# Kernel tuning notes

Measured on AMD Instinct MI355X. Metric: run time of the kernel, lower is better.

## Reference

```python
import jax, jax.numpy as jnp
import numpy as np

EMBED_DIM = 1024
NUM_HEADS = 16
D_K = EMBED_DIM // NUM_HEADS


def setup_inputs() -> dict:
    key = jax.random.key(0)
    ks = jax.random.split(key, 5)
    s = 1.0 / np.sqrt(EMBED_DIM)  # roughly match nn.Linear init scale
    return {
        "x": jax.random.normal(ks[0], (2, 2048, EMBED_DIM), dtype=jnp.float32),
        "wq": jax.random.normal(ks[1], (EMBED_DIM, EMBED_DIM), dtype=jnp.float32) * s,
        "wk": jax.random.normal(ks[2], (EMBED_DIM, EMBED_DIM), dtype=jnp.float32) * s,
        "wv": jax.random.normal(ks[3], (EMBED_DIM, EMBED_DIM), dtype=jnp.float32) * s,
        "wo": jax.random.normal(ks[4], (EMBED_DIM, EMBED_DIM), dtype=jnp.float32) * s,
    }


def reference(x, wq, wk, wv, wo):
    b, s, e = x.shape
    # nn.Linear(bias=False): y = x @ W.T
    def split_heads(t):
        return t.reshape(b, s, NUM_HEADS, D_K).transpose(0, 2, 1, 3)  # [b,h,s,d]
    q = split_heads(x @ wq.T)
    k = split_heads(x @ wk.T)
    v = split_heads(x @ wv.T)
    scores = jnp.einsum("bhqd,bhkd->bhqk", q, k) / jnp.sqrt(jnp.float32(D_K))
    attn = jax.nn.softmax(scores, axis=-1)
    out = jnp.einsum("bhqk,bhkd->bhqd", attn, v)  # [b,h,s,d]
    out = out.transpose(0, 2, 1, 3).reshape(b, s, e)
    return out @ wo.T
```

## Files before the change

kernel.cpp:

```cpp
#include <hip/hip_runtime.h>
#include <stdint.h>

typedef unsigned short u16;
typedef float f32x4 __attribute__((ext_vector_type(4)));
typedef __bf16 bf16x8 __attribute__((ext_vector_type(8)));

__device__ __forceinline__ u16 f2bf(float f) {
  union { float f; uint32_t u; } c; c.f = f;
  uint32_t u = c.u;
  u += 0x7fffu + ((u >> 16) & 1u);
  return (u16)(u >> 16);
}

#define GLOAD_LDS16(g, l)                                                              \
  __builtin_amdgcn_global_load_lds((__attribute__((address_space(1))) void*)(g),       \
                                   (__attribute__((address_space(3))) void*)(l), 16, 0, 0)

__global__ __launch_bounds__(256) void cvt_all(const float* __restrict__ x,
                                               const float* __restrict__ wq,
                                               const float* __restrict__ wk,
                                               const float* __restrict__ wv,
                                               const float* __restrict__ wo,
                                               u16* __restrict__ xb,
                                               u16* __restrict__ wqkvb,
                                               u16* __restrict__ wob) {
  int bx = blockIdx.x;
  const float* src;
  u16* dst;
  int i;
  if (bx < 4096) {
    src = x; dst = xb; i = bx * 256 + threadIdx.x;
  } else {
    int r = bx - 4096;
    int w = r >> 10;
    i = (r & 1023) * 256 + threadIdx.x;
    if (w == 0)      { src = wq; dst = wqkvb; }
    else if (w == 1) { src = wk; dst = wqkvb + 1048576; }
    else if (w == 2) { src = wv; dst = wqkvb + 2097152; }
    else             { src = wo; dst = wob; }
  }
  const float4 v = ((const float4*)src)[i];
  ushort4 o;
  o.x = f2bf(v.x); o.y = f2bf(v.y); o.z = f2bf(v.z); o.w = f2bf(v.w);
  ((ushort4*)dst)[i] = o;
}

__global__ __launch_bounds__(256) void gemm_qkv(const u16* __restrict__ A,
                                                const u16* __restrict__ B,
                                                u16* __restrict__ QKb,
                                                u16* __restrict__ Vt) {
  const int K = 1024;
  __shared__ __align__(16) u16 sA[128 * 32];
  __shared__ __align__(16) u16 sB[128 * 32];
  const int tid = threadIdx.x;
  const int lane = tid & 63;
  const int wave = tid >> 6;
  const int quad = lane >> 4, l16 = lane & 15;
  const int wm = (wave >> 1) * 64, wn = (wave & 1) * 64;
  const int bm = blockIdx.y * 128, bn = blockIdx.x * 128;

  const int ar = tid >> 2;
  const int ac = (tid & 3) * 8;

  f32x4 acc[4][4];
#pragma unroll
  for (int i = 0; i < 4; i++)
#pragma unroll
    for (int j = 0; j < 4; j++) acc[i][j] = (f32x4){0.f, 0.f, 0.f, 0.f};

  const u16* pA0 = A + (size_t)(bm + ar) * K + ac;
  const u16* pA1 = A + (size_t)(bm + 64 + ar) * K + ac;
  const u16* pB0 = B + (size_t)(bn + ar) * K + ac;
  const u16* pB1 = B + (size_t)(bn + 64 + ar) * K + ac;

  for (int k0 = 0; k0 < K; k0 += 32) {
    GLOAD_LDS16(pA0 + k0, (char*)sA + tid * 16);
    GLOAD_LDS16(pA1 + k0, (char*)sA + 4096 + tid * 16);
    GLOAD_LDS16(pB0 + k0, (char*)sB + tid * 16);
    GLOAD_LDS16(pB1 + k0, (char*)sB + 4096 + tid * 16);
    __syncthreads();
    bf16x8 af[4], bfr[4];
#pragma unroll
    for (int mt = 0; mt < 4; mt++)
      af[mt] = *(const bf16x8*)&sA[(wm + mt * 16 + l16) * 32 + quad * 8];
#pragma unroll
    for (int nt = 0; nt < 4; nt++)
      bfr[nt] = *(const bf16x8*)&sB[(wn + nt * 16 + l16) * 32 + quad * 8];
#pragma unroll
    for (int mt = 0; mt < 4; mt++)
#pragma unroll
      for (int nt = 0; nt < 4; nt++)
        acc[mt][nt] = __builtin_amdgcn_mfma_f32_16x16x32_bf16(af[mt], bfr[nt], acc[mt][nt], 0, 0, 0);
    __syncthreads();
  }

  if (blockIdx.x < 16) {
    const float qs = (blockIdx.x < 8) ? 0.125f : 1.0f;
#pragma unroll
    for (int mt = 0; mt < 4; mt++)
#pragma unroll
      for (int nt = 0; nt < 4; nt++)
#pragma unroll
        for (int r = 0; r < 4; r++) {
          int row = bm + wm + mt * 16 + quad * 4 + r;
          int col = bn + wn + nt * 16 + l16;
          QKb[(size_t)row * 2048 + col] = f2bf(acc[mt][nt][r] * qs);
        }
  } else {
#pragma unroll
    for (int mt = 0; mt < 4; mt++)
#pragma unroll
      for (int nt = 0; nt < 4; nt++) {
        int hd = (bn - 2048) + wn + nt * 16 + l16;
        int tok = bm + wm + mt * 16 + quad * 4;
        ushort4 o;
        o.x = f2bf(acc[mt][nt][0]);
        o.y = f2bf(acc[mt][nt][1]);
        o.z = f2bf(acc[mt][nt][2]);
        o.w = f2bf(acc[mt][nt][3]);
        *(ushort4*)&Vt[(size_t)hd * 4096 + tok] = o;
      }
  }
}

__global__ __launch_bounds__(256, 2) void attn_fwd(const u16* __restrict__ QKb,
                                                   const u16* __restrict__ Vt,
                                                   u16* __restrict__ O) {
  const int qt = blockIdx.x, h = blockIdx.y, b = blockIdx.z;
  const int tid = threadIdx.x;
  const int lane = tid & 63;
  const int wave = tid >> 6;
  const int quad = lane >> 4, l16 = lane & 15;
  const int qh = wave >> 1;
  const int kvh = wave & 1;

  __shared__ __align__(16) u16 sK[2][128 * 64];
  __shared__ __align__(16) u16 sV[2][64 * 128];
  __shared__ __align__(16) u16 sQP[8192];

  const int tok0 = b * 2048;
  const int q0 = qt * 128;
  const int colh = h * 64;

#pragma unroll
  for (int k2 = 0; k2 < 4; k2++) {
    int c = k2 * 256 + tid;
    int row = c >> 3, c8 = (c & 7) ^ (row & 7);
    GLOAD_LDS16(QKb + (size_t)(tok0 + q0 + row) * 2048 + colh + c8 * 8,
                (char*)sQP + c * 16);
  }
#pragma unroll
  for (int k2 = 0; k2 < 4; k2++) {
    int c = k2 * 256 + tid;
    int rowk = c >> 3, c8 = (c & 7) ^ (rowk & 7);
    GLOAD_LDS16(QKb + (size_t)(tok0 + rowk) * 2048 + 1024 + colh + c8 * 8,
                (char*)sK[0] + c * 16);
    int rowv = c >> 4, c16 = (c & 15) ^ (rowv & 15);
    GLOAD_LDS16(Vt + (size_t)(colh + rowv) * 4096 + tok0 + c16 * 8,
                (char*)sV[0] + c * 16);
  }
  __syncthreads();

  bf16x8 aq[4][2];
#pragma unroll
  for (int sub = 0; sub < 4; sub++)
#pragma unroll
    for (int kh = 0; kh < 2; kh++) {
      int row = qh * 64 + sub * 16 + l16;
      aq[sub][kh] = *(const bf16x8*)&sQP[row * 64 + (((kh * 4 + quad) ^ (row & 7)) * 8)];
    }
  __syncthreads();

  u16* sP = sQP + wave * 1152;

  f32x4 oacc[4][4];
  float lsum[4][4];
#pragma unroll
  for (int sub = 0; sub < 4; sub++)
#pragma unroll
    for (int nt = 0; nt < 4; nt++) oacc[sub][nt] = (f32x4){0.f, 0.f, 0.f, 0.f};
#pragma unroll
  for (int sub = 0; sub < 4; sub++)
#pragma unroll
    for (int r = 0; r < 4; r++) lsum[sub][r] = 0.f;

  int p = 0;
  for (int it = 0; it < 16; ++it) {
    const int nkv = (it < 15 ? it + 1 : 15) * 128;
#pragma unroll
    for (int k2 = 0; k2 < 4; k2++) {
      int c = k2 * 256 + tid;
      int rowk = c >> 3, c8 = (c & 7) ^ (rowk & 7);
      GLOAD_LDS16(QKb + (size_t)(tok0 + nkv + rowk) * 2048 + 1024 + colh + c8 * 8,
                  (char*)sK[p ^ 1] + c * 16);
      int rowv = c >> 4, c16 = (c & 15) ^ (rowv & 15);
      GLOAD_LDS16(Vt + (size_t)(colh + rowv) * 4096 + tok0 + nkv + c16 * 8,
                  (char*)sV[p ^ 1] + c * 16);
    }

    bf16x8 kf[4][2], vf[4][2];
#pragma unroll
    for (int nt = 0; nt < 4; nt++)
#pragma unroll
      for (int kh = 0; kh < 2; kh++) {
        int rk = kvh * 64 + nt * 16 + l16;
        kf[nt][kh] = *(const bf16x8*)&sK[p][rk * 64 + (((kh * 4 + quad) ^ (rk & 7)) * 8)];
        int rv = nt * 16 + l16;
        vf[nt][kh] = *(const bf16x8*)&sV[p][rv * 128 + (((kvh * 8 + kh * 4 + quad) ^ (rv & 15)) * 8)];
      }

#pragma unroll
    for (int sub = 0; sub < 4; sub++) {
      f32x4 sc[4];
#pragma unroll
      for (int nt = 0; nt < 4; nt++) {
        f32x4 c = (f32x4){0.f, 0.f, 0.f, 0.f};
        c = __builtin_amdgcn_mfma_f32_16x16x32_bf16(aq[sub][0], kf[nt][0], c, 0, 0, 0);
        c = __builtin_amdgcn_mfma_f32_16x16x32_bf16(aq[sub][1], kf[nt][1], c, 0, 0, 0);
        sc[nt] = c;
      }
#pragma unroll
      for (int nt = 0; nt < 4; nt++)
#pragma unroll
        for (int r = 0; r < 4; r++) {
          union { float f; uint32_t u; } cc;
          cc.f = __expf(sc[nt][r]);
          sP[(quad * 4 + r) * 72 + nt * 16 + l16] = (u16)(cc.u >> 16);
          cc.u &= 0xffff0000u;
          lsum[sub][r] += cc.f;
        }
      bf16x8 ap0 = *(const bf16x8*)&sP[l16 * 72 + quad * 8];
      bf16x8 ap1 = *(const bf16x8*)&sP[l16 * 72 + 32 + quad * 8];
#pragma unroll
      for (int nt = 0; nt < 4; nt++) {
        oacc[sub][nt] = __builtin_amdgcn_mfma_f32_16x16x32_bf16(ap0, vf[nt][0], oacc[sub][nt], 0, 0, 0);
        oacc[sub][nt] = __builtin_amdgcn_mfma_f32_16x16x32_bf16(ap1, vf[nt][1], oacc[sub][nt], 0, 0, 0);
      }
    }
    __syncthreads();
    p ^= 1;
  }

#pragma unroll
  for (int sub = 0; sub < 4; sub++)
#pragma unroll
    for (int r = 0; r < 4; r++) {
      float v = lsum[sub][r];
#pragma unroll
      for (int m = 1; m < 16; m <<= 1) v += __shfl_xor(v, m, 64);
      lsum[sub][r] = v;
    }

  float* mO = (float*)sK;
  float* mL = (float*)sV;
  if (kvh == 1) {
#pragma unroll
    for (int sub = 0; sub < 4; sub++)
#pragma unroll
      for (int nt = 0; nt < 4; nt++)
#pragma unroll
        for (int r = 0; r < 4; r++)
          mO[qh * 4096 + (sub * 16 + quad * 4 + r) * 64 + nt * 16 + l16] = oacc[sub][nt][r];
    if (l16 == 0)
#pragma unroll
      for (int sub = 0; sub < 4; sub++)
#pragma unroll
        for (int r = 0; r < 4; r++)
          mL[qh * 64 + sub * 16 + quad * 4 + r] = lsum[sub][r];
  }
  __syncthreads();
  if (kvh == 0) {
#pragma unroll
    for (int sub = 0; sub < 4; sub++)
#pragma unroll
      for (int r = 0; r < 4; r++) {
        int ql = sub * 16 + quad * 4 + r;
        float inv = 1.0f / (lsum[sub][r] + mL[qh * 64 + ql]);
        int row = tok0 + q0 + qh * 64 + ql;
#pragma unroll
        for (int nt = 0; nt < 4; nt++) {
          float o = oacc[sub][nt][r] + mO[qh * 4096 + ql * 64 + nt * 16 + l16];
          O[(size_t)row * 1024 + colh + nt * 16 + l16] = f2bf(o * inv);
        }
      }
  }
}

__global__ __launch_bounds__(256) void gemm_out(const u16* __restrict__ A,
                                                const u16* __restrict__ B,
                                                float* __restrict__ C) {
  const int N = 1024, K = 1024;
  __shared__ __align__(16) u16 sA[128 * 32];
  __shared__ __align__(16) u16 sB[64 * 32];
  const int tid = threadIdx.x;
  const int lane = tid & 63;
  const int wave = tid >> 6;
  const int quad = lane >> 4, l16 = lane & 15;
  const int wm = (wave >> 1) * 64, wn = (wave & 1) * 32;
  const int bm = blockIdx.y * 128, bn = blockIdx.x * 64;
  const int ar = tid >> 2;
  const int ac = (tid & 3) * 8;

  f32x4 acc[4][2];
#pragma unroll
  for (int i = 0; i < 4; i++)
#pragma unroll
    for (int j = 0; j < 2; j++) acc[i][j] = (f32x4){0.f, 0.f, 0.f, 0.f};

  const u16* pA0 = A + (size_t)(bm + ar) * K + ac;
  const u16* pA1 = A + (size_t)(bm + 64 + ar) * K + ac;
  const u16* pB0 = B + (size_t)(bn + ar) * K + ac;

  for (int k0 = 0; k0 < K; k0 += 32) {
    GLOAD_LDS16(pA0 + k0, (char*)sA + tid * 16);
    GLOAD_LDS16(pA1 + k0, (char*)sA + 4096 + tid * 16);
    GLOAD_LDS16(pB0 + k0, (char*)sB + tid * 16);
    __syncthreads();
    bf16x8 af[4], bfr[2];
#pragma unroll
    for (int mt = 0; mt < 4; mt++)
      af[mt] = *(const bf16x8*)&sA[(wm + mt * 16 + l16) * 32 + quad * 8];
#pragma unroll
    for (int nt = 0; nt < 2; nt++)
      bfr[nt] = *(const bf16x8*)&sB[(wn + nt * 16 + l16) * 32 + quad * 8];
#pragma unroll
    for (int mt = 0; mt < 4; mt++)
#pragma unroll
      for (int nt = 0; nt < 2; nt++)
        acc[mt][nt] = __builtin_amdgcn_mfma_f32_16x16x32_bf16(af[mt], bfr[nt], acc[mt][nt], 0, 0, 0);
    __syncthreads();
  }

#pragma unroll
  for (int mt = 0; mt < 4; mt++)
#pragma unroll
    for (int nt = 0; nt < 2; nt++)
#pragma unroll
      for (int r = 0; r < 4; r++) {
        int row = bm + wm + mt * 16 + quad * 4 + r;
        int col = bn + wn + nt * 16 + l16;
        C[(size_t)row * N + col] = acc[mt][nt][r];
      }
}

extern "C" void kernel_launch(void* const* d_in, const int* in_sizes, int n_in,
                              void* d_out, int out_size, void* d_ws, size_t ws_size,
                              hipStream_t stream) {
  const float* x  = (const float*)d_in[0];
  const float* wq = (const float*)d_in[1];
  const float* wk = (const float*)d_in[2];
  const float* wv = (const float*)d_in[3];
  const float* wo = (const float*)d_in[4];
  float* out = (float*)d_out;
  char* ws = (char*)d_ws;
  const size_t MB = 1u << 20;

  u16* xb    = (u16*)(ws);
  u16* wqkvb = (u16*)(ws + 8 * MB);
  u16* wob   = (u16*)(ws + 14 * MB);
  u16* QKb   = (u16*)(ws + 16 * MB);
  u16* Vtb   = (u16*)(ws + 32 * MB);
  u16* Ob    = xb;

  cvt_all<<<8192, 256, 0, stream>>>(x, wq, wk, wv, wo, xb, wqkvb, wob);

  gemm_qkv<<<dim3(24, 32), 256, 0, stream>>>(xb, wqkvb, QKb, Vtb);

  attn_fwd<<<dim3(16, 16, 2), 256, 0, stream>>>(QKb, Vtb, Ob);

  gemm_out<<<dim3(16, 32), 256, 0, stream>>>(Ob, wob, out);
}
```

Baseline: 211.7 us.

## Restructure attention: per-wave query rows, transposed MFMA, register P via shuffles

Rewrites the attention kernel so each wave owns 32 query rows over the full KV range with 64-token KV tiles, and drops the split-KV merge through shared memory. It swaps the MFMA operand order so scores land transposed, packs exp values to bf16 with perm and redistributes them through lane shuffles instead of an LDS round-trip for P. It also shrinks LDS to raise occupancy to 3 blocks, linearizes the grid, and stages output through LDS for 16-byte stores. The cost is more shuffle traffic and more loop iterations with more barriers. The packing step changes bf16 rounding of the row sums slightly.

```diff
diff --git a/kernel.cpp b/kernel.cpp
--- a/kernel.cpp
+++ b/kernel.cpp
@@ -10,6 +10,11 @@
   uint32_t u = c.u;
   u += 0x7fffu + ((u >> 16) & 1u);
   return (u16)(u >> 16);
+}
+
+__device__ __forceinline__ uint32_t pkbf(float a, float b) {
+  union { float f; uint32_t u; } ua, ub; ua.f = a; ub.f = b;
+  return __builtin_amdgcn_perm(ub.u, ua.u, 0x07060302u);
 }
 
 #define GLOAD_LDS16(g, l)                                                              \
@@ -123,20 +128,24 @@
   }
 }
 
-__global__ __launch_bounds__(256, 2) void attn_fwd(const u16* __restrict__ QKb,
+__global__ __launch_bounds__(256, 3) void attn_fwd(const u16* __restrict__ QKb,
                                                    const u16* __restrict__ Vt,
                                                    u16* __restrict__ O) {
-  const int qt = blockIdx.x, h = blockIdx.y, b = blockIdx.z;
+  const int bx = blockIdx.x;
+  const int qt = bx >> 5;
+  const int h  = (bx >> 1) & 15;
+  const int b  = bx & 1;
   const int tid = threadIdx.x;
   const int lane = tid & 63;
   const int wave = tid >> 6;
   const int quad = lane >> 4, l16 = lane & 15;
-  const int qh = wave >> 1;
-  const int kvh = wave & 1;
-
-  __shared__ __align__(16) u16 sK[2][128 * 64];
-  __shared__ __align__(16) u16 sV[2][64 * 128];
-  __shared__ __align__(16) u16 sQP[8192];
+
+  __shared__ __align__(16) u16 smem[24576];
+  u16* sK0 = smem;
+  u16* sK1 = smem + 4096;
+  u16* sV0 = smem + 8192;
+  u16* sV1 = smem + 12288;
+  u16* sQ  = smem + 16384;
 
   const int tok0 = b * 2048;
   const int q0 = qt * 128;
@@ -147,55 +156,56 @@
     int c = k2 * 256 + tid;
     int row = c >> 3, c8 = (c & 7) ^ (row & 7);
     GLOAD_LDS16(QKb + (size_t)(tok0 + q0 + row) * 2048 + colh + c8 * 8,
-                (char*)sQP + c * 16);
-  }
-#pragma unroll
-  for (int k2 = 0; k2 < 4; k2++) {
+                (char*)sQ + c * 16);
+  }
+#pragma unroll
+  for (int k2 = 0; k2 < 2; k2++) {
     int c = k2 * 256 + tid;
-    int rowk = c >> 3, c8 = (c & 7) ^ (rowk & 7);
-    GLOAD_LDS16(QKb + (size_t)(tok0 + rowk) * 2048 + 1024 + colh + c8 * 8,
-                (char*)sK[0] + c * 16);
-    int rowv = c >> 4, c16 = (c & 15) ^ (rowv & 15);
-    GLOAD_LDS16(Vt + (size_t)(colh + rowv) * 4096 + tok0 + c16 * 8,
-                (char*)sV[0] + c * 16);
+    int row = c >> 3, c8 = (c & 7) ^ (row & 7);
+    GLOAD_LDS16(QKb + (size_t)(tok0 + row) * 2048 + 1024 + colh + c8 * 8,
+                (char*)sK0 + c * 16);
+    GLOAD_LDS16(Vt + (size_t)(colh + row) * 4096 + tok0 + c8 * 8,
+                (char*)sV0 + c * 16);
   }
   __syncthreads();
 
-  bf16x8 aq[4][2];
-#pragma unroll
-  for (int sub = 0; sub < 4; sub++)
+  bf16x8 aq[2][2];
+#pragma unroll
+  for (int sub = 0; sub < 2; sub++)
 #pragma unroll
     for (int kh = 0; kh < 2; kh++) {
-      int row = qh * 64 + sub * 16 + l16;
-      aq[sub][kh] = *(const bf16x8*)&sQP[row * 64 + (((kh * 4 + quad) ^ (row & 7)) * 8)];
+      int row = wave * 32 + sub * 16 + l16;
+      aq[sub][kh] = *(const bf16x8*)&sQ[row * 64 + (((kh * 4 + quad) ^ (row & 7)) * 8)];
     }
-  __syncthreads();
-
-  u16* sP = sQP + wave * 1152;
-
-  f32x4 oacc[4][4];
-  float lsum[4][4];
-#pragma unroll
-  for (int sub = 0; sub < 4; sub++)
+
+  f32x4 oacc[2][4];
+  float lsum[2] = {0.f, 0.f};
+#pragma unroll
+  for (int sub = 0; sub < 2; sub++)
 #pragma unroll
     for (int nt = 0; nt < 4; nt++) oacc[sub][nt] = (f32x4){0.f, 0.f, 0.f, 0.f};
-#pragma unroll
-  for (int sub = 0; sub < 4; sub++)
-#pragma unroll
-    for (int r = 0; r < 4; r++) lsum[sub][r] = 0.f;
+
+  const int srcA = ((quad & 1) * 32 + l16);
+  const int srcB = srcA + 16;
+  const bool hiT = (quad >= 2);
 
   int p = 0;
-  for (int it = 0; it < 16; ++it) {
-    const int nkv = (it < 15 ? it + 1 : 15) * 128;
-#pragma unroll
-    for (int k2 = 0; k2 < 4; k2++) {
-      int c = k2 * 256 + tid;
-      int rowk = c >> 3, c8 = (c & 7) ^ (rowk & 7);
-      GLOAD_LDS16(QKb + (size_t)(tok0 + nkv + rowk) * 2048 + 1024 + colh + c8 * 8,
-                  (char*)sK[p ^ 1] + c * 16);
-      int rowv = c >> 4, c16 = (c & 15) ^ (rowv & 15);
-      GLOAD_LDS16(Vt + (size_t)(colh + rowv) * 4096 + tok0 + nkv + c16 * 8,
-                  (char*)sV[p ^ 1] + c * 16);
+  for (int it = 0; it < 32; ++it) {
+    u16* sKc = p ? sK1 : sK0;
+    u16* sVc = p ? sV1 : sV0;
+    if (it < 31) {
+      u16* sKn = p ? sK0 : sK1;
+      u16* sVn = p ? sV0 : sV1;
+      const int nkv = (it + 1) * 64;
+#pragma unroll
+      for (int k2 = 0; k2 < 2; k2++) {
+        int c = k2 * 256 + tid;
+        int row = c >> 3, c8 = (c & 7) ^ (row & 7);
+        GLOAD_LDS16(QKb + (size_t)(tok0 + nkv + row) * 2048 + 1024 + colh + c8 * 8,
+                    (char*)sKn + c * 16);
+        GLOAD_LDS16(Vt + (size_t)(colh + row) * 4096 + tok0 + nkv + c8 * 8,
+                    (char*)sVn + c * 16);
+      }
     }
 
     bf16x8 kf[4][2], vf[4][2];
@@ -203,38 +213,46 @@
     for (int nt = 0; nt < 4; nt++)
 #pragma unroll
       for (int kh = 0; kh < 2; kh++) {
-        int rk = kvh * 64 + nt * 16 + l16;
-        kf[nt][kh] = *(const bf16x8*)&sK[p][rk * 64 + (((kh * 4 + quad) ^ (rk & 7)) * 8)];
-        int rv = nt * 16 + l16;
-        vf[nt][kh] = *(const bf16x8*)&sV[p][rv * 128 + (((kvh * 8 + kh * 4 + quad) ^ (rv & 15)) * 8)];
-      }
-
-#pragma unroll
-    for (int sub = 0; sub < 4; sub++) {
-      f32x4 sc[4];
+        int rr = nt * 16 + l16;
+        int off = rr * 64 + (((kh * 4 + quad) ^ (rr & 7)) * 8);
+        kf[nt][kh] = *(const bf16x8*)&sKc[off];
+        vf[nt][kh] = *(const bf16x8*)&sVc[off];
+      }
+
+#pragma unroll
+    for (int sub = 0; sub < 2; sub++) {
+      f32x4 e[4];
 #pragma unroll
       for (int nt = 0; nt < 4; nt++) {
         f32x4 c = (f32x4){0.f, 0.f, 0.f, 0.f};
-        c = __builtin_amdgcn_mfma_f32_16x16x32_bf16(aq[sub][0], kf[nt][0], c, 0, 0, 0);
-        c = __builtin_amdgcn_mfma_f32_16x16x32_bf16(aq[sub][1], kf[nt][1], c, 0, 0, 0);
-        sc[nt] = c;
-      }
-#pragma unroll
-      for (int nt = 0; nt < 4; nt++)
-#pragma unroll
-        for (int r = 0; r < 4; r++) {
-          union { float f; uint32_t u; } cc;
-          cc.f = __expf(sc[nt][r]);
-          sP[(quad * 4 + r) * 72 + nt * 16 + l16] = (u16)(cc.u >> 16);
-          cc.u &= 0xffff0000u;
-          lsum[sub][r] += cc.f;
-        }
-      bf16x8 ap0 = *(const bf16x8*)&sP[l16 * 72 + quad * 8];
-      bf16x8 ap1 = *(const bf16x8*)&sP[l16 * 72 + 32 + quad * 8];
-#pragma unroll
-      for (int nt = 0; nt < 4; nt++) {
-        oacc[sub][nt] = __builtin_amdgcn_mfma_f32_16x16x32_bf16(ap0, vf[nt][0], oacc[sub][nt], 0, 0, 0);
-        oacc[sub][nt] = __builtin_amdgcn_mfma_f32_16x16x32_bf16(ap1, vf[nt][1], oacc[sub][nt], 0, 0, 0);
+        c = __builtin_amdgcn_mfma_f32_16x16x32_bf16(kf[nt][0], aq[sub][0], c, 0, 0, 0);
+        c = __builtin_amdgcn_mfma_f32_16x16x32_bf16(kf[nt][1], aq[sub][1], c, 0, 0, 0);
+#pragma unroll
+        for (int r = 0; r < 4; r++) e[nt][r] = __expf(c[r]);
+        lsum[sub] += (e[nt][0] + e[nt][1]) + (e[nt][2] + e[nt][3]);
+      }
+#pragma unroll
+      for (int kh = 0; kh < 2; kh++) {
+        uint32_t pk0 = pkbf(e[2 * kh][0], e[2 * kh][1]);
+        uint32_t pk1 = pkbf(e[2 * kh][2], e[2 * kh][3]);
+        uint32_t pk2_ = pkbf(e[2 * kh + 1][0], e[2 * kh + 1][1]);
+        uint32_t pk3_ = pkbf(e[2 * kh + 1][2], e[2 * kh + 1][3]);
+        uint32_t a0 = (uint32_t)__shfl((int)pk0, srcA, 64);
+        uint32_t c0 = (uint32_t)__shfl((int)pk2_, srcA, 64);
+        uint32_t a1 = (uint32_t)__shfl((int)pk1, srcA, 64);
+        uint32_t c1 = (uint32_t)__shfl((int)pk3_, srcA, 64);
+        uint32_t a2 = (uint32_t)__shfl((int)pk0, srcB, 64);
+        uint32_t c2 = (uint32_t)__shfl((int)pk2_, srcB, 64);
+        uint32_t a3 = (uint32_t)__shfl((int)pk1, srcB, 64);
+        uint32_t c3 = (uint32_t)__shfl((int)pk3_, srcB, 64);
+        union { uint32_t u[4]; bf16x8 v; } bb;
+        bb.u[0] = hiT ? c0 : a0;
+        bb.u[1] = hiT ? c1 : a1;
+        bb.u[2] = hiT ? c2 : a2;
+        bb.u[3] = hiT ? c3 : a3;
+#pragma unroll
+        for (int nt = 0; nt < 4; nt++)
+          oacc[sub][nt] = __builtin_amdgcn_mfma_f32_16x16x32_bf16(vf[nt][kh], bb.v, oacc[sub][nt], 0, 0, 0);
       }
     }
     __syncthreads();
@@ -242,47 +260,28 @@
   }
 
 #pragma unroll
-  for (int sub = 0; sub < 4; sub++)
-#pragma unroll
-    for (int r = 0; r < 4; r++) {
-      float v = lsum[sub][r];
-#pragma unroll
-      for (int m = 1; m < 16; m <<= 1) v += __shfl_xor(v, m, 64);
-      lsum[sub][r] = v;
-    }
-
-  float* mO = (float*)sK;
-  float* mL = (float*)sV;
-  if (kvh == 1) {
-#pragma unroll
-    for (int sub = 0; sub < 4; sub++)
-#pragma unroll
-      for (int nt = 0; nt < 4; nt++)
-#pragma unroll
-        for (int r = 0; r < 4; r++)
-          mO[qh * 4096 + (sub * 16 + quad * 4 + r) * 64 + nt * 16 + l16] = oacc[sub][nt][r];
-    if (l16 == 0)
-#pragma unroll
-      for (int sub = 0; sub < 4; sub++)
-#pragma unroll
-        for (int r = 0; r < 4; r++)
-          mL[qh * 64 + sub * 16 + quad * 4 + r] = lsum[sub][r];
-  }
-  __syncthreads();
-  if (kvh == 0) {
-#pragma unroll
-    for (int sub = 0; sub < 4; sub++)
-#pragma unroll
-      for (int r = 0; r < 4; r++) {
-        int ql = sub * 16 + quad * 4 + r;
-        float inv = 1.0f / (lsum[sub][r] + mL[qh * 64 + ql]);
-        int row = tok0 + q0 + qh * 64 + ql;
-#pragma unroll
-        for (int nt = 0; nt < 4; nt++) {
-          float o = oacc[sub][nt][r] + mO[qh * 4096 + ql * 64 + nt * 16 + l16];
-          O[(size_t)row * 1024 + colh + nt * 16 + l16] = f2bf(o * inv);
-        }
-      }
+  for (int sub = 0; sub < 2; sub++) {
+    float v = lsum[sub];
+    v += __shfl_xor(v, 16, 64);
+    v += __shfl_xor(v, 32, 64);
+    lsum[sub] = 1.0f / v;
+  }
+
+  u16* sT = smem + wave * 6144;
+#pragma unroll
+  for (int sub = 0; sub < 2; sub++)
+#pragma unroll
+    for (int nt = 0; nt < 4; nt++)
+#pragma unroll
+      for (int r = 0; r < 4; r++)
+        sT[(sub * 16 + l16) * 68 + nt * 16 + quad * 4 + r] = f2bf(oacc[sub][nt][r] * lsum[sub]);
+#pragma unroll
+  for (int k = 0; k < 4; k++) {
+    int qrow = k * 8 + (lane >> 3);
+    int cch = lane & 7;
+    uint4 vrow = *(const uint4*)&sT[qrow * 68 + cch * 8];
+    int tokr = tok0 + q0 + wave * 32 + qrow;
+    *(uint4*)&O[(size_t)tokr * 1024 + colh + cch * 8] = vrow;
   }
 }
 
@@ -366,7 +365,7 @@
 
   gemm_qkv<<<dim3(24, 32), 256, 0, stream>>>(xb, wqkvb, QKb, Vtb);
 
-  attn_fwd<<<dim3(16, 16, 2), 256, 0, stream>>>(QKb, Vtb, Ob);
+  attn_fwd<<<512, 256, 0, stream>>>(QKb, Vtb, Ob);
 
   gemm_out<<<dim3(16, 32), 256, 0, stream>>>(Ob, wob, out);
 }
```

New measurement: 204.9 us. -3.2%, faster.
